# Performance work log

Hardware: AMD Instinct MI355X
Metric: run time of the kernel (lower is better)

Reference implementation:

```python
import jax, jax.numpy as jnp
import numpy as np

EMBED = 512
HEADS = 8
HEAD_DIM = EMBED // HEADS
SCALE_BASE = 512
NEG = -1e9


def xpos_apply(x, offset, downscale):
    # x: [(b h), L, d]
    L, d = x.shape[1], x.shape[2]
    min_pos = -(L + offset) // 2
    max_pos = L + offset + min_pos
    base = (jnp.arange(0, d, 2, dtype=jnp.float32) + 0.4 * d) / (1.4 * d)      # [d/2]
    power = jnp.arange(min_pos, max_pos, dtype=jnp.float32) / SCALE_BASE        # [L']
    scale = base[None, :] ** power[:, None]                                     # [L', d/2]
    half = d // 2
    inv_freq = 1.0 / (10000.0 ** (jnp.arange(half, dtype=jnp.float32) / half))
    sinusoid = jnp.arange(scale.shape[0], dtype=jnp.float32)[:, None] * inv_freq[None, :]
    sin, cos = jnp.sin(sinusoid), jnp.cos(sinusoid)
    # keep last L rows (no-op when offset == 0)
    scale, sin, cos = scale[-L:], sin[-L:], cos[-L:]
    if downscale:
        scale = 1.0 / scale
    sin2 = jnp.repeat(sin * scale, 2, axis=-1)   # duplicate_interleave -> [L, d]
    cos2 = jnp.repeat(cos * scale, 2, axis=-1)
    x1, x2 = x[..., ::2], x[..., 1::2]
    rot = jnp.stack([-x2, x1], axis=-1).reshape(x.shape)  # rotate_every_two
    return x * cos2[None] + rot * sin2[None]


def split_heads(x, b, L):
    # 'b l (h d) -> (b h) l d'
    return x.reshape(b, L, HEADS, HEAD_DIM).transpose(0, 2, 1, 3).reshape(b * HEADS, L, HEAD_DIM)


def setup_inputs() -> dict:
    key = jax.random.key(0)
    ks = jax.random.split(key, 12)
    b, L = 4, 2048
    inp = {
        'query': jax.random.normal(ks[0], (b, L, EMBED), jnp.float32),
        'key': jax.random.normal(ks[1], (b, L, EMBED), jnp.float32),
        'value': jax.random.normal(ks[2], (b, L, EMBED), jnp.float32),
        'key_padding_mask': jnp.zeros((b, L), jnp.bool_),
        'attn_mask': jnp.where(jnp.tril(jnp.ones((L, L), jnp.bool_)), 0.0, NEG).astype(jnp.float32),
    }
    s = 1.0 / np.sqrt(EMBED)
    inp['Wq'] = jax.random.normal(ks[3], (EMBED, EMBED), jnp.float32) * s
    inp['bq'] = jnp.zeros((EMBED,), jnp.float32)
    inp['Wk'] = jax.random.normal(ks[4], (EMBED, EMBED), jnp.float32) * s
    inp['bk'] = jnp.zeros((EMBED,), jnp.float32)
    inp['Wv'] = jax.random.normal(ks[5], (EMBED, EMBED), jnp.float32) * s
    inp['bv'] = jnp.zeros((EMBED,), jnp.float32)
    inp['Wo'] = jax.random.normal(ks[6], (EMBED, EMBED), jnp.float32) * s
    inp['bo'] = jnp.zeros((EMBED,), jnp.float32)
    return inp


def reference(query, key, value, key_padding_mask, attn_mask, Wq, bq, Wk, bk, Wv, bv, Wo, bo):
    b, L, _ = query.shape
    q = split_heads(query @ Wq.T + bq, b, L)
    k = split_heads(key @ Wk.T + bk, b, L)
    v = split_heads(value @ Wv.T + bv, b, L)
    k = xpos_apply(k, 0, True)
    q = xpos_apply(q, 0, False)
    q = q * (HEAD_DIM ** -0.5)
    aw = jnp.einsum('btd,bsd->bts', q, k)                 # [(b h), t, s]
    aw = jnp.nan_to_num(aw) + attn_mask[None]
    aw = aw.reshape(b, HEADS, L, L)
    aw = jnp.where(key_padding_mask[:, None, None, :], jnp.finfo(aw.dtype).min, aw)
    aw = aw.reshape(b * HEADS, L, L)
    probs = jax.nn.softmax(aw.astype(jnp.float32), axis=-1).astype(aw.dtype)
    attn = jnp.einsum('bts,bsd->btd', probs, v)           # [(b h), t, d]
    attn = attn.reshape(b, HEADS, L, HEAD_DIM).transpose(0, 2, 1, 3).reshape(b, L, EMBED)
    return attn @ Wo.T + bo
```

## Files before the change

### kernel.cpp

```cpp
#include <hip/hip_runtime.h>
#include <hip/hip_bf16.h>

typedef __bf16 bf16x2 __attribute__((ext_vector_type(2)));
typedef __bf16 bf16x4 __attribute__((ext_vector_type(4)));
typedef __bf16 bf16x8 __attribute__((ext_vector_type(8)));
typedef float  f32x4  __attribute__((ext_vector_type(4)));

#define SEQ    2048
#define EMB    512
#define NHEAD  8
#define HD     64
#define NBATCH 4
#define MROWS  (NBATCH*SEQ)
#define QSCALE 0.18033688011112042f
#define INV2PI 0.15915494309189535f
#define TWOPI  6.28318530717958648f
#define NEGFREQ (-0.41524101186092028f)

__device__ __forceinline__ f32x4 mfma16(bf16x8 a, bf16x8 b, f32x4 c) {
  return __builtin_amdgcn_mfma_f32_16x16x32_bf16(a, b, c, 0, 0, 0);
}

typedef __attribute__((address_space(1))) const void gv_t;
typedef __attribute__((address_space(3))) void lv_t;
__device__ __forceinline__ void async16(const void* g, void* l) {
  __builtin_amdgcn_global_load_lds((gv_t*)g, (lv_t*)l, 16, 0, 0);
}

__global__ __launch_bounds__(256) void conv_kernel(const float* __restrict__ q,
                                                   const float* __restrict__ k,
                                                   const float* __restrict__ v,
                                                   __bf16* __restrict__ Qf,
                                                   __bf16* __restrict__ Kf,
                                                   __bf16* __restrict__ Vf) {
  const int z = blockIdx.y;
  const float* src = (z == 0) ? q : (z == 1) ? k : v;
  __bf16* dst = (z == 0) ? Qf : (z == 1) ? Kf : Vf;
  const size_t i8 = ((size_t)blockIdx.x * 256 + threadIdx.x) * 8;
  const float4 fa = ((const float4*)(src + i8))[0];
  const float4 fb = ((const float4*)(src + i8))[1];
  bf16x8 h = { (__bf16)fa.x, (__bf16)fa.y, (__bf16)fa.z, (__bf16)fa.w,
               (__bf16)fb.x, (__bf16)fb.y, (__bf16)fb.z, (__bf16)fb.w };
  *(bf16x8*)(dst + i8) = h;
}

__device__ __forceinline__ void gemm_main(const __bf16* __restrict__ A,
                                          const float* __restrict__ W,
                                          __bf16* As, __bf16* Bs,
                                          f32x4 (&acc)[4][4], int m0, int n0) {
  const int tid = threadIdx.x;
  const int wid = tid >> 6, lane = tid & 63;
  const int quad = lane >> 4, l16 = lane & 15;
  const int srow = lane >> 3;
  const int sxor = ((lane & 7) ^ srow) * 8;
  const int wm = (wid >> 1) * 64, wn = (wid & 1) * 64;

  #pragma unroll
  for (int i = 0; i < 4; ++i)
    #pragma unroll
    for (int j = 0; j < 4; ++j) acc[i][j] = (f32x4)(0.0f);

  for (int k0 = 0; k0 < 512; k0 += 64) {
    __syncthreads();
    #pragma unroll
    for (int ii = 0; ii < 4; ++ii) {
      const int r8 = wid * 32 + ii * 8;
      async16(A + (size_t)(m0 + r8 + srow) * 512 + k0 + sxor, &As[r8 * 64]);
    }
    {
      const int row = tid >> 1, c0 = (tid & 1) << 5;
      const float* src = W + (size_t)(n0 + row) * 512 + k0 + c0;
      __bf16* dst = Bs + row * 72 + c0;
      #pragma unroll
      for (int j = 0; j < 4; ++j) {
        const float4 fa = ((const float4*)src)[2 * j];
        const float4 fb = ((const float4*)src)[2 * j + 1];
        bf16x8 h = { (__bf16)fa.x, (__bf16)fa.y, (__bf16)fa.z, (__bf16)fa.w,
                     (__bf16)fb.x, (__bf16)fb.y, (__bf16)fb.z, (__bf16)fb.w };
        *((bf16x8*)(dst + 8 * j)) = h;
      }
    }
    __syncthreads();
    #pragma unroll
    for (int ks = 0; ks < 2; ++ks) {
      bf16x8 af[4], bfr[4];
      #pragma unroll
      for (int i = 0; i < 4; ++i)
        af[i] = *(const bf16x8*)&As[(wm + i * 16 + l16) * 64 +
                                    (((quad + ks * 4) ^ (l16 & 7)) * 8)];
      #pragma unroll
      for (int j = 0; j < 4; ++j)
        bfr[j] = *(const bf16x8*)&Bs[(wn + j * 16 + l16) * 72 + ks * 32 + quad * 8];
      #pragma unroll
      for (int i = 0; i < 4; ++i)
        #pragma unroll
        for (int j = 0; j < 4; ++j)
          acc[i][j] = mfma16(af[i], bfr[j], acc[i][j]);
    }
  }
}

__global__ __launch_bounds__(256) void gemm_proj_kernel(
    const __bf16* __restrict__ Qf, const __bf16* __restrict__ Kf, const __bf16* __restrict__ Vf,
    const float* __restrict__ wq, const float* __restrict__ wk, const float* __restrict__ wv,
    const float* __restrict__ bq, const float* __restrict__ bk, const float* __restrict__ bv,
    __bf16* __restrict__ Qx, __bf16* __restrict__ Kx, __bf16* __restrict__ Vt) {
  __shared__ __align__(16) char smem[34816];
  __bf16* As = (__bf16*)smem;
  __bf16* Bs = (__bf16*)(smem + 16384);
  __bf16* T  = (__bf16*)smem;

  const int z = blockIdx.z;
  const __bf16* A = (z == 0) ? Qf : (z == 1) ? Kf : Vf;
  const float* W  = (z == 0) ? wq : (z == 1) ? wk : wv;
  const float* bias = (z == 0) ? bq : (z == 1) ? bk : bv;
  const int m0 = blockIdx.y * 128, n0 = blockIdx.x * 128;

  f32x4 acc[4][4];
  gemm_main(A, W, As, Bs, acc, m0, n0);

  const int tid = threadIdx.x;
  const int wid = tid >> 6, lane = tid & 63;
  const int quad = lane >> 4, l16 = lane & 15;
  const int wm = (wid >> 1) * 64, wn = (wid & 1) * 64;

  __syncthreads();

  if (z == 2) {
    #pragma unroll
    for (int j = 0; j < 4; ++j) {
      const float bval = bias[n0 + wn + j * 16 + l16];
      #pragma unroll
      for (int i = 0; i < 4; ++i) {
        bf16x4 p = { (__bf16)(acc[i][j][0] + bval), (__bf16)(acc[i][j][1] + bval),
                     (__bf16)(acc[i][j][2] + bval), (__bf16)(acc[i][j][3] + bval) };
        *(bf16x4*)&T[(wn + j * 16 + l16) * 136 + wm + i * 16 + quad * 4] = p;
      }
    }
    __syncthreads();
    const int nrow = tid >> 1, mh = (tid & 1) << 6;
    bf16x8 vv[8];
    #pragma unroll
    for (int u = 0; u < 8; ++u) vv[u] = *(const bf16x8*)&T[nrow * 136 + mh + u * 8];
    const int n = n0 + nrow, h = n >> 6, d = n & 63;
    const int bb = m0 >> 11, lb2 = (m0 & 2047) + mh;
    __bf16* dst = Vt + ((size_t)(bb * 8 + h) * 64 + d) * 2048 + lb2;
    #pragma unroll
    for (int u = 0; u < 8; ++u) *(bf16x8*)(dst + u * 8) = vv[u];
  } else {
    #pragma unroll
    for (int j = 0; j < 4; ++j) {
      const float bval = bias[n0 + wn + j * 16 + l16];
      #pragma unroll
      for (int i = 0; i < 4; ++i)
        #pragma unroll
        for (int r = 0; r < 4; ++r)
          T[(wm + i * 16 + quad * 4 + r) * 136 + wn + j * 16 + l16] =
              (__bf16)(acc[i][j][r] + bval);
    }
    __syncthreads();
    const int lrow = tid >> 1, half = tid & 1;
    const int gm = m0 + lrow, l = gm & 2047, bb = gm >> 11;
    const int h = (n0 >> 6) + half;
    bf16x8 vv[8];
    #pragma unroll
    for (int u = 0; u < 8; ++u)
      vv[u] = *(const bf16x8*)&T[lrow * 136 + half * 64 + u * 8];
    bf16x8 ov[8];
    const float lf = (float)l;
    const float pw = (lf - 1024.0f) * (1.0f / 512.0f);
    const float qs = (z == 0) ? QSCALE : 1.0f;
    #pragma unroll
    for (int i = 0; i < 32; ++i) {
      const float x1 = (float)vv[i >> 2][(2 * i) & 7];
      const float x2 = (float)vv[i >> 2][(2 * i + 1) & 7];
      const float lb = __log2f((2.0f * i + 25.6f) * (1.0f / 89.6f));
      const float e  = (z == 0) ? (pw * lb) : (-pw * lb);
      const float sc = __builtin_amdgcn_exp2f(e) * qs;
      const float ang = lf * __builtin_amdgcn_exp2f((float)i * NEGFREQ);
      float rev = ang * INV2PI;
      rev -= floorf(rev);
      const float ar = rev * TWOPI;
      const float sn = __sinf(ar) * sc;
      const float cs = __cosf(ar) * sc;
      ov[i >> 2][(2 * i) & 7]     = (__bf16)(x1 * cs - x2 * sn);
      ov[i >> 2][(2 * i + 1) & 7] = (__bf16)(x2 * cs + x1 * sn);
    }
    __bf16* dst = ((z == 0) ? Qx : Kx) + ((size_t)(bb * 8 + h) * 2048 + l) * 64;
    #pragma unroll
    for (int u = 0; u < 8; ++u) *(bf16x8*)(dst + u * 8) = ov[u];
  }
}

__global__ __launch_bounds__(256) void gemm_out_kernel(
    const __bf16* __restrict__ A, const float* __restrict__ W,
    const float* __restrict__ bias, float* __restrict__ C) {
  __shared__ __align__(16) char smem[34816];
  __bf16* As = (__bf16*)smem;
  __bf16* Bs = (__bf16*)(smem + 16384);
  const int m0 = blockIdx.y * 128, n0 = blockIdx.x * 128;
  f32x4 acc[4][4];
  gemm_main(A, W, As, Bs, acc, m0, n0);
  const int tid = threadIdx.x;
  const int wid = tid >> 6, lane = tid & 63;
  const int quad = lane >> 4, l16 = lane & 15;
  const int wm = (wid >> 1) * 64, wn = (wid & 1) * 64;
  #pragma unroll
  for (int j = 0; j < 4; ++j) {
    const int n = n0 + wn + j * 16 + l16;
    const float bval = bias[n];
    #pragma unroll
    for (int i = 0; i < 4; ++i)
      #pragma unroll
      for (int r = 0; r < 4; ++r)
        C[(size_t)(m0 + wm + i * 16 + quad * 4 + r) * 512 + n] = acc[i][j][r] + bval;
  }
}

__global__ __launch_bounds__(256) void flash_kernel(const __bf16* __restrict__ Qx,
                                                    const __bf16* __restrict__ Kx,
                                                    const __bf16* __restrict__ Vt,
                                                    const unsigned char* __restrict__ kpm,
                                                    __bf16* __restrict__ Oa) {
  __shared__ __align__(16) __bf16 Qs[64 * HD];
  __shared__ __align__(16) __bf16 Ks[64 * HD];
  __shared__ __align__(16) __bf16 Vs[64 * HD];
  __shared__ __align__(16) __bf16 Ps[4][16 * 72];

  const int tid = threadIdx.x;
  const int wid = tid >> 6;
  const int lane = tid & 63;
  const int quad = lane >> 4;
  const int l16 = lane & 15;
  const int srow = lane >> 3;
  const int sxor = ((lane & 7) ^ srow) * 8;
  const int l7 = l16 & 7;
  const int bh = blockIdx.x;
  const int b = bh >> 3;
  const int qb = 31 - (int)blockIdx.y;
  const int q0 = qb * 64;

  const __bf16* Qbase = Qx + (size_t)bh * (SEQ * HD);
  const __bf16* Kbase = Kx + (size_t)bh * (SEQ * HD);
  const __bf16* Vbase = Vt + (size_t)bh * (HD * SEQ);
  __bf16* Pw = &Ps[wid][0];

  #pragma unroll
  for (int ii = 0; ii < 2; ++ii) {
    const int r0 = wid * 16 + ii * 8;
    async16(Qbase + (size_t)(q0 + r0 + srow) * HD + sxor, &Qs[r0 * HD]);
  }
  __syncthreads();
  const bf16x8 qf0 = *(const bf16x8*)&Qs[(wid * 16 + l16) * HD + ((quad ^ l7) * 8)];
  const bf16x8 qf1 = *(const bf16x8*)&Qs[(wid * 16 + l16) * HD + (((quad + 4) ^ l7) * 8)];

  f32x4 o0 = (f32x4)(0.0f), o1 = (f32x4)(0.0f), o2 = (f32x4)(0.0f), o3 = (f32x4)(0.0f);
  float m_run = -1e30f, l_run = 0.0f;
  const int myq = q0 + wid * 16 + l16;

  for (int kv0 = 0; kv0 < q0 + 64; kv0 += 64) {
    __syncthreads();
    #pragma unroll
    for (int ii = 0; ii < 2; ++ii) {
      const int r0 = wid * 16 + ii * 8;
      async16(Kbase + (size_t)(kv0 + r0 + srow) * HD + sxor, &Ks[r0 * HD]);
      async16(Vbase + (size_t)(r0 + srow) * SEQ + kv0 + sxor, &Vs[r0 * HD]);
    }
    __syncthreads();

    f32x4 s[4];
    #pragma unroll
    for (int nb = 0; nb < 4; ++nb) s[nb] = (f32x4)(0.0f);
    #pragma unroll
    for (int nb = 0; nb < 4; ++nb) {
      const bf16x8 kf = *(const bf16x8*)&Ks[(nb * 16 + l16) * HD + ((quad ^ l7) * 8)];
      s[nb] = mfma16(kf, qf0, s[nb]);
    }
    #pragma unroll
    for (int nb = 0; nb < 4; ++nb) {
      const bf16x8 kf = *(const bf16x8*)&Ks[(nb * 16 + l16) * HD + (((quad + 4) ^ l7) * 8)];
      s[nb] = mfma16(kf, qf1, s[nb]);
    }

    if (kv0 + 63 > q0 + wid * 16) {
      #pragma unroll
      for (int nb = 0; nb < 4; ++nb)
        #pragma unroll
        for (int r = 0; r < 4; ++r)
          if (kv0 + nb * 16 + quad * 4 + r > myq) s[nb][r] = -1e30f;
    }
    {
      const unsigned char* kp0 = kpm + b * SEQ + kv0;
      #pragma unroll
      for (int nb = 0; nb < 4; ++nb) {
        const unsigned pk = *(const unsigned*)(kp0 + nb * 16 + quad * 4);
        if (pk) {
          if (pk & 0x000000FFu) s[nb][0] = -1e30f;
          if (pk & 0x0000FF00u) s[nb][1] = -1e30f;
          if (pk & 0x00FF0000u) s[nb][2] = -1e30f;
          if (pk & 0xFF000000u) s[nb][3] = -1e30f;
        }
      }
    }

    float mx = s[0][0];
    #pragma unroll
    for (int nb = 0; nb < 4; ++nb)
      #pragma unroll
      for (int r = 0; r < 4; ++r) mx = fmaxf(mx, s[nb][r]);
    mx = fmaxf(mx, __shfl_xor(mx, 16));
    mx = fmaxf(mx, __shfl_xor(mx, 32));
    const float m_new = fmaxf(m_run, mx);
    const float alpha = __builtin_amdgcn_exp2f(m_run - m_new);
    m_run = m_new;
    float ssum = 0.0f;
    #pragma unroll
    for (int nb = 0; nb < 4; ++nb) {
      #pragma unroll
      for (int r = 0; r < 4; ++r) {
        const float p = __builtin_amdgcn_exp2f(s[nb][r] - m_new);
        s[nb][r] = p;
        ssum += p;
      }
    }
    ssum += __shfl_xor(ssum, 16);
    ssum += __shfl_xor(ssum, 32);
    l_run = l_run * alpha + ssum;

    #pragma unroll
    for (int nb = 0; nb < 4; ++nb) {
      bf16x4 p4 = { (__bf16)s[nb][0], (__bf16)s[nb][1],
                    (__bf16)s[nb][2], (__bf16)s[nb][3] };
      *(bf16x4*)&Pw[l16 * 72 + nb * 16 + quad * 4] = p4;
    }
    o0 *= alpha; o1 *= alpha; o2 *= alpha; o3 *= alpha;

    #pragma unroll
    for (int ks = 0; ks < 2; ++ks) {
      const bf16x8 pf = *(const bf16x8*)&Pw[l16 * 72 + ks * 32 + quad * 8];
      const int bx = ((quad + ks * 4) ^ l7) * 8;
      o0 = mfma16(*(const bf16x8*)&Vs[( 0 + l16) * HD + bx], pf, o0);
      o1 = mfma16(*(const bf16x8*)&Vs[(16 + l16) * HD + bx], pf, o1);
      o2 = mfma16(*(const bf16x8*)&Vs[(32 + l16) * HD + bx], pf, o2);
      o3 = mfma16(*(const bf16x8*)&Vs[(48 + l16) * HD + bx], pf, o3);
    }
  }

  const float inv_l = 1.0f / l_run;
  {
    bf16x4 t0 = { (__bf16)(o0[0] * inv_l), (__bf16)(o0[1] * inv_l),
                  (__bf16)(o0[2] * inv_l), (__bf16)(o0[3] * inv_l) };
    bf16x4 t1 = { (__bf16)(o1[0] * inv_l), (__bf16)(o1[1] * inv_l),
                  (__bf16)(o1[2] * inv_l), (__bf16)(o1[3] * inv_l) };
    bf16x4 t2 = { (__bf16)(o2[0] * inv_l), (__bf16)(o2[1] * inv_l),
                  (__bf16)(o2[2] * inv_l), (__bf16)(o2[3] * inv_l) };
    bf16x4 t3 = { (__bf16)(o3[0] * inv_l), (__bf16)(o3[1] * inv_l),
                  (__bf16)(o3[2] * inv_l), (__bf16)(o3[3] * inv_l) };
    *(bf16x4*)&Pw[l16 * 72 +  0 + quad * 4] = t0;
    *(bf16x4*)&Pw[l16 * 72 + 16 + quad * 4] = t1;
    *(bf16x4*)&Pw[l16 * 72 + 32 + quad * 4] = t2;
    *(bf16x4*)&Pw[l16 * 72 + 48 + quad * 4] = t3;
  }
  const int h = bh & 7;
  #pragma unroll
  for (int ii = 0; ii < 2; ++ii) {
    const int qr = ii * 8 + (lane >> 3);
    const bf16x8 ovv = *(const bf16x8*)&Pw[qr * 72 + (lane & 7) * 8];
    *(bf16x8*)(Oa + (((size_t)b * SEQ + q0 + wid * 16 + qr) * NHEAD + h) * HD +
               (lane & 7) * 8) = ovv;
  }
}

extern "C" void kernel_launch(void* const* d_in, const int* in_sizes, int n_in,
                              void* d_out, int out_size, void* d_ws, size_t ws_size,
                              hipStream_t stream) {
  (void)in_sizes; (void)n_in; (void)out_size; (void)ws_size;
  const float* query = (const float*)d_in[0];
  const float* key   = (const float*)d_in[1];
  const float* value = (const float*)d_in[2];
  const unsigned char* kpm = (const unsigned char*)d_in[3];
  const float* Wq = (const float*)d_in[5];
  const float* bq = (const float*)d_in[6];
  const float* Wk = (const float*)d_in[7];
  const float* bk = (const float*)d_in[8];
  const float* Wv = (const float*)d_in[9];
  const float* bv = (const float*)d_in[10];
  const float* Wo = (const float*)d_in[11];
  const float* bo = (const float*)d_in[12];
  float* out = (float*)d_out;

  char* ws = (char*)d_ws;
  const size_t SZ = (size_t)MROWS * EMB * 2;
  __bf16* Qf = (__bf16*)(ws);
  __bf16* Kf = (__bf16*)(ws + SZ);
  __bf16* Vf = (__bf16*)(ws + 2 * SZ);
  __bf16* Qx = (__bf16*)(ws + 3 * SZ);
  __bf16* Kx = (__bf16*)(ws + 4 * SZ);
  __bf16* Vt = (__bf16*)(ws + 5 * SZ);
  __bf16* Oa = Qf;

  conv_kernel<<<dim3(2048, 3), dim3(256), 0, stream>>>(query, key, value, Qf, Kf, Vf);
  gemm_proj_kernel<<<dim3(4, 64, 3), dim3(256), 0, stream>>>(
      Qf, Kf, Vf, Wq, Wk, Wv, bq, bk, bv, Qx, Kx, Vt);
  flash_kernel<<<dim3(32, 32), dim3(256), 0, stream>>>(Qx, Kx, Vt, kpm, Oa);
  gemm_out_kernel<<<dim3(4, 64), dim3(256), 0, stream>>>(Oa, Wo, bo, out);
}
```

Before: 233.3 us.

## Pair causal query blocks per workgroup and double-buffer K/V tiles in flash kernel

Each flash workgroup now processes two query blocks (31-t and t), so every block does exactly 33 KV iterations. This balances the causal triangle and halves the grid. K/V tiles are double-buffered, with the next tile's async load issued before computing the current one, which removes one barrier per iteration. The key padding mask is staged once into shared memory. In exchange, LDS use and register pressure rise, and the grid shrinks to 512 blocks, which may lower occupancy.

```diff
diff --git a/kernel.cpp b/kernel.cpp
--- a/kernel.cpp
+++ b/kernel.cpp
@@ -222,23 +222,26 @@
                                                     const __bf16* __restrict__ Vt,
                                                     const unsigned char* __restrict__ kpm,
                                                     __bf16* __restrict__ Oa) {
-  __shared__ __align__(16) __bf16 Qs[64 * HD];
-  __shared__ __align__(16) __bf16 Ks[64 * HD];
-  __shared__ __align__(16) __bf16 Vs[64 * HD];
+  __shared__ __align__(16) __bf16 Qs[2][64 * HD];
+  __shared__ __align__(16) __bf16 Ks[2][64 * HD];
+  __shared__ __align__(16) __bf16 Vs[2][64 * HD];
   __shared__ __align__(16) __bf16 Ps[4][16 * 72];
+  __shared__ __align__(16) unsigned char kpmS[2048];
 
   const int tid = threadIdx.x;
   const int wid = tid >> 6;
   const int lane = tid & 63;
   const int quad = lane >> 4;
   const int l16 = lane & 15;
+  const int l7 = l16 & 7;
   const int srow = lane >> 3;
   const int sxor = ((lane & 7) ^ srow) * 8;
-  const int l7 = l16 & 7;
   const int bh = blockIdx.x;
-  const int b = bh >> 3;
-  const int qb = 31 - (int)blockIdx.y;
-  const int q0 = qb * 64;
+  const int b = bh >> 3, h = bh & 7;
+  const int t = blockIdx.y;
+  const int qb0 = 31 - t, qb1 = t;
+  const int n0 = qb0 + 1;
+  const int ntot = n0 + qb1 + 1;
 
   const __bf16* Qbase = Qx + (size_t)bh * (SEQ * HD);
   const __bf16* Kbase = Kx + (size_t)bh * (SEQ * HD);
@@ -246,108 +249,33 @@
   __bf16* Pw = &Ps[wid][0];
 
   #pragma unroll
+  for (int p = 0; p < 2; ++p) {
+    const int q0p = (p ? qb1 : qb0) * 64;
+    #pragma unroll
+    for (int ii = 0; ii < 2; ++ii) {
+      const int r0 = wid * 16 + ii * 8;
+      async16(Qbase + (size_t)(q0p + r0 + srow) * HD + sxor, &Qs[p][r0 * HD]);
+    }
+  }
+  if (wid < 2) async16(kpm + b * SEQ + tid * 16, &kpmS[tid * 16]);
+  #pragma unroll
   for (int ii = 0; ii < 2; ++ii) {
     const int r0 = wid * 16 + ii * 8;
-    async16(Qbase + (size_t)(q0 + r0 + srow) * HD + sxor, &Qs[r0 * HD]);
+    async16(Kbase + (size_t)(r0 + srow) * HD + sxor, &Ks[0][r0 * HD]);
+    async16(Vbase + (size_t)(r0 + srow) * SEQ + sxor, &Vs[0][r0 * HD]);
   }
   __syncthreads();
-  const bf16x8 qf0 = *(const bf16x8*)&Qs[(wid * 16 + l16) * HD + ((quad ^ l7) * 8)];
-  const bf16x8 qf1 = *(const bf16x8*)&Qs[(wid * 16 + l16) * HD + (((quad + 4) ^ l7) * 8)];
+
+  bf16x8 qf0 = *(const bf16x8*)&Qs[0][(wid * 16 + l16) * HD + ((quad ^ l7) * 8)];
+  bf16x8 qf1 = *(const bf16x8*)&Qs[0][(wid * 16 + l16) * HD + (((quad + 4) ^ l7) * 8)];
 
   f32x4 o0 = (f32x4)(0.0f), o1 = (f32x4)(0.0f), o2 = (f32x4)(0.0f), o3 = (f32x4)(0.0f);
-  float m_run = -1e30f, l_run = 0.0f;
-  const int myq = q0 + wid * 16 + l16;
-
-  for (int kv0 = 0; kv0 < q0 + 64; kv0 += 64) {
-    __syncthreads();
-    #pragma unroll
-    for (int ii = 0; ii < 2; ++ii) {
-      const int r0 = wid * 16 + ii * 8;
-      async16(Kbase + (size_t)(kv0 + r0 + srow) * HD + sxor, &Ks[r0 * HD]);
-      async16(Vbase + (size_t)(r0 + srow) * SEQ + kv0 + sxor, &Vs[r0 * HD]);
-    }
-    __syncthreads();
-
-    f32x4 s[4];
-    #pragma unroll
-    for (int nb = 0; nb < 4; ++nb) s[nb] = (f32x4)(0.0f);
-    #pragma unroll
-    for (int nb = 0; nb < 4; ++nb) {
-      const bf16x8 kf = *(const bf16x8*)&Ks[(nb * 16 + l16) * HD + ((quad ^ l7) * 8)];
-      s[nb] = mfma16(kf, qf0, s[nb]);
-    }
-    #pragma unroll
-    for (int nb = 0; nb < 4; ++nb) {
-      const bf16x8 kf = *(const bf16x8*)&Ks[(nb * 16 + l16) * HD + (((quad + 4) ^ l7) * 8)];
-      s[nb] = mfma16(kf, qf1, s[nb]);
-    }
-
-    if (kv0 + 63 > q0 + wid * 16) {
-      #pragma unroll
-      for (int nb = 0; nb < 4; ++nb)
-        #pragma unroll
-        for (int r = 0; r < 4; ++r)
-          if (kv0 + nb * 16 + quad * 4 + r > myq) s[nb][r] = -1e30f;
-    }
-    {
-      const unsigned char* kp0 = kpm + b * SEQ + kv0;
-      #pragma unroll
-      for (int nb = 0; nb < 4; ++nb) {
-        const unsigned pk = *(const unsigned*)(kp0 + nb * 16 + quad * 4);
-        if (pk) {
-          if (pk & 0x000000FFu) s[nb][0] = -1e30f;
-          if (pk & 0x0000FF00u) s[nb][1] = -1e30f;
-          if (pk & 0x00FF0000u) s[nb][2] = -1e30f;
-          if (pk & 0xFF000000u) s[nb][3] = -1e30f;
-        }
-      }
-    }
-
-    float mx = s[0][0];
-    #pragma unroll
-    for (int nb = 0; nb < 4; ++nb)
-      #pragma unroll
-      for (int r = 0; r < 4; ++r) mx = fmaxf(mx, s[nb][r]);
-    mx = fmaxf(mx, __shfl_xor(mx, 16));
-    mx = fmaxf(mx, __shfl_xor(mx, 32));
-    const float m_new = fmaxf(m_run, mx);
-    const float alpha = __builtin_amdgcn_exp2f(m_run - m_new);
-    m_run = m_new;
-    float ssum = 0.0f;
-    #pragma unroll
-    for (int nb = 0; nb < 4; ++nb) {
-      #pragma unroll
-      for (int r = 0; r < 4; ++r) {
-        const float p = __builtin_amdgcn_exp2f(s[nb][r] - m_new);
-        s[nb][r] = p;
-        ssum += p;
-      }
-    }
-    ssum += __shfl_xor(ssum, 16);
-    ssum += __shfl_xor(ssum, 32);
-    l_run = l_run * alpha + ssum;
-
-    #pragma unroll
-    for (int nb = 0; nb < 4; ++nb) {
-      bf16x4 p4 = { (__bf16)s[nb][0], (__bf16)s[nb][1],
-                    (__bf16)s[nb][2], (__bf16)s[nb][3] };
-      *(bf16x4*)&Pw[l16 * 72 + nb * 16 + quad * 4] = p4;
-    }
-    o0 *= alpha; o1 *= alpha; o2 *= alpha; o3 *= alpha;
-
-    #pragma unroll
-    for (int ks = 0; ks < 2; ++ks) {
-      const bf16x8 pf = *(const bf16x8*)&Pw[l16 * 72 + ks * 32 + quad * 8];
-      const int bx = ((quad + ks * 4) ^ l7) * 8;
-      o0 = mfma16(*(const bf16x8*)&Vs[( 0 + l16) * HD + bx], pf, o0);
-      o1 = mfma16(*(const bf16x8*)&Vs[(16 + l16) * HD + bx], pf, o1);
-      o2 = mfma16(*(const bf16x8*)&Vs[(32 + l16) * HD + bx], pf, o2);
-      o3 = mfma16(*(const bf16x8*)&Vs[(48 + l16) * HD + bx], pf, o3);
-    }
-  }
-
-  const float inv_l = 1.0f / l_run;
-  {
+  float m_run = -3.0e38f, l_run = 0.0f;
+  int qb = qb0, q0 = qb0 * 64;
+  int myq = q0 + wid * 16 + l16;
+
+  auto store_O = [&](int q0s) {
+    const float inv_l = 1.0f / l_run;
     bf16x4 t0 = { (__bf16)(o0[0] * inv_l), (__bf16)(o0[1] * inv_l),
                   (__bf16)(o0[2] * inv_l), (__bf16)(o0[3] * inv_l) };
     bf16x4 t1 = { (__bf16)(o1[0] * inv_l), (__bf16)(o1[1] * inv_l),
@@ -360,15 +288,116 @@
     *(bf16x4*)&Pw[l16 * 72 + 16 + quad * 4] = t1;
     *(bf16x4*)&Pw[l16 * 72 + 32 + quad * 4] = t2;
     *(bf16x4*)&Pw[l16 * 72 + 48 + quad * 4] = t3;
-  }
-  const int h = bh & 7;
-  #pragma unroll
-  for (int ii = 0; ii < 2; ++ii) {
-    const int qr = ii * 8 + (lane >> 3);
-    const bf16x8 ovv = *(const bf16x8*)&Pw[qr * 72 + (lane & 7) * 8];
-    *(bf16x8*)(Oa + (((size_t)b * SEQ + q0 + wid * 16 + qr) * NHEAD + h) * HD +
-               (lane & 7) * 8) = ovv;
-  }
+    #pragma unroll
+    for (int ii = 0; ii < 2; ++ii) {
+      const int qr = ii * 8 + srow;
+      const bf16x8 ovv = *(const bf16x8*)&Pw[qr * 72 + (lane & 7) * 8];
+      *(bf16x8*)(Oa + (((size_t)b * SEQ + q0s + wid * 16 + qr) * NHEAD + h) * HD +
+                 (lane & 7) * 8) = ovv;
+    }
+  };
+
+  for (int i = 0; i < 33; ++i) {
+    const int buf = i & 1;
+    if (i + 1 < ntot) {
+      const int inext = i + 1;
+      const int kvn = (inext < n0) ? inext : (inext - n0);
+      #pragma unroll
+      for (int ii = 0; ii < 2; ++ii) {
+        const int r0 = wid * 16 + ii * 8;
+        async16(Kbase + (size_t)(kvn * 64 + r0 + srow) * HD + sxor, &Ks[buf ^ 1][r0 * HD]);
+        async16(Vbase + (size_t)(r0 + srow) * SEQ + kvn * 64 + sxor, &Vs[buf ^ 1][r0 * HD]);
+      }
+    }
+    if (i == n0) {
+      store_O(qb0 * 64);
+      qf0 = *(const bf16x8*)&Qs[1][(wid * 16 + l16) * HD + ((quad ^ l7) * 8)];
+      qf1 = *(const bf16x8*)&Qs[1][(wid * 16 + l16) * HD + (((quad + 4) ^ l7) * 8)];
+      o0 = o1 = o2 = o3 = (f32x4)(0.0f);
+      m_run = -3.0e38f; l_run = 0.0f;
+      qb = qb1; q0 = qb1 * 64; myq = q0 + wid * 16 + l16;
+    }
+    if (i >= ntot) { __syncthreads(); continue; }
+    const int kv = (i < n0) ? i : (i - n0);
+
+    f32x4 s[4];
+    #pragma unroll
+    for (int nb = 0; nb < 4; ++nb) s[nb] = (f32x4)(0.0f);
+    #pragma unroll
+    for (int nb = 0; nb < 4; ++nb) {
+      const bf16x8 kf = *(const bf16x8*)&Ks[buf][(nb * 16 + l16) * HD + ((quad ^ l7) * 8)];
+      s[nb] = mfma16(kf, qf0, s[nb]);
+    }
+    #pragma unroll
+    for (int nb = 0; nb < 4; ++nb) {
+      const bf16x8 kf = *(const bf16x8*)&Ks[buf][(nb * 16 + l16) * HD + (((quad + 4) ^ l7) * 8)];
+      s[nb] = mfma16(kf, qf1, s[nb]);
+    }
+
+    if (kv == qb) {
+      #pragma unroll
+      for (int nb = 0; nb < 4; ++nb)
+        #pragma unroll
+        for (int r = 0; r < 4; ++r)
+          if (kv * 64 + nb * 16 + quad * 4 + r > myq) s[nb][r] = -1e30f;
+    }
+    #pragma unroll
+    for (int nb = 0; nb < 4; ++nb) {
+      const unsigned pk = *(const unsigned*)&kpmS[kv * 64 + nb * 16 + quad * 4];
+      if (pk) {
+        if (pk & 0x000000FFu) s[nb][0] = -1e30f;
+        if (pk & 0x0000FF00u) s[nb][1] = -1e30f;
+        if (pk & 0x00FF0000u) s[nb][2] = -1e30f;
+        if (pk & 0xFF000000u) s[nb][3] = -1e30f;
+      }
+    }
+
+    float mx = s[0][0];
+    #pragma unroll
+    for (int nb = 0; nb < 4; ++nb)
+      #pragma unroll
+      for (int r = 0; r < 4; ++r) mx = fmaxf(mx, s[nb][r]);
+    mx = fmaxf(mx, __shfl_xor(mx, 16));
+    mx = fmaxf(mx, __shfl_xor(mx, 32));
+    const float m_new = fmaxf(m_run, mx);
+    const float alpha = __builtin_amdgcn_exp2f(m_run - m_new);
+    m_run = m_new;
+    float ssum = 0.0f;
+    #pragma unroll
+    for (int nb = 0; nb < 4; ++nb) {
+      #pragma unroll
+      for (int r = 0; r < 4; ++r) {
+        const float p = __builtin_amdgcn_exp2f(s[nb][r] - m_new);
+        s[nb][r] = p;
+        ssum += p;
+      }
+    }
+    ssum += __shfl_xor(ssum, 16);
+    ssum += __shfl_xor(ssum, 32);
+    l_run = l_run * alpha + ssum;
+
+    #pragma unroll
+    for (int nb = 0; nb < 4; ++nb) {
+      bf16x4 p4 = { (__bf16)s[nb][0], (__bf16)s[nb][1],
+                    (__bf16)s[nb][2], (__bf16)s[nb][3] };
+      *(bf16x4*)&Pw[l16 * 72 + nb * 16 + quad * 4] = p4;
+    }
+    o0 *= alpha; o1 *= alpha; o2 *= alpha; o3 *= alpha;
+
+    #pragma unroll
+    for (int ks = 0; ks < 2; ++ks) {
+      const bf16x8 pf = *(const bf16x8*)&Pw[l16 * 72 + ks * 32 + quad * 8];
+      const int bx = ((quad + ks * 4) ^ l7) * 8;
+      o0 = mfma16(*(const bf16x8*)&Vs[buf][( 0 + l16) * HD + bx], pf, o0);
+      o1 = mfma16(*(const bf16x8*)&Vs[buf][(16 + l16) * HD + bx], pf, o1);
+      o2 = mfma16(*(const bf16x8*)&Vs[buf][(32 + l16) * HD + bx], pf, o2);
+      o3 = mfma16(*(const bf16x8*)&Vs[buf][(48 + l16) * HD + bx], pf, o3);
+    }
+
+    __syncthreads();
+  }
+
+  store_O(qb1 * 64);
 }
 
 extern "C" void kernel_launch(void* const* d_in, const int* in_sizes, int n_in,
@@ -402,6 +431,6 @@
   conv_kernel<<<dim3(2048, 3), dim3(256), 0, stream>>>(query, key, value, Qf, Kf, Vf);
   gemm_proj_kernel<<<dim3(4, 64, 3), dim3(256), 0, stream>>>(
       Qf, Kf, Vf, Wq, Wk, Wv, bq, bk, bv, Qx, Kx, Vt);
-  flash_kernel<<<dim3(32, 32), dim3(256), 0, stream>>>(Qx, Kx, Vt, kpm, Oa);
+  flash_kernel<<<dim3(32, 16), dim3(256), 0, stream>>>(Qx, Kx, Vt, kpm, Oa);
   gemm_out_kernel<<<dim3(4, 64), dim3(256), 0, stream>>>(Oa, Wo, bo, out);
 }
```

Measured after the change: 227.9 us. -2.3%, faster.

## Use 128-row query tiles in flash attention with reordered scheduling and staged padding mask

Applied to the files above, without the earlier changes.

The flash attention kernel now gives each block 128 query rows (32 per wave, two 16-row MFMA column groups), so every K/V tile loaded into shared memory feeds twice as many MFMAs and the grid halves. The key padding mask is staged once into shared memory, and the first K/V tile is prefetched together with Q. Query tiles are scheduled in a mixed order (largest first, then smallest) to balance the causal workload. The larger tile raises register pressure, which the launch bounds try to contain, and leaves fewer blocks to spread across CUs.

```diff
diff --git a/kernel.cpp b/kernel.cpp
--- a/kernel.cpp
+++ b/kernel.cpp
@@ -217,28 +217,31 @@
   }
 }
 
-__global__ __launch_bounds__(256) void flash_kernel(const __bf16* __restrict__ Qx,
-                                                    const __bf16* __restrict__ Kx,
-                                                    const __bf16* __restrict__ Vt,
-                                                    const unsigned char* __restrict__ kpm,
-                                                    __bf16* __restrict__ Oa) {
-  __shared__ __align__(16) __bf16 Qs[64 * HD];
+__global__ __launch_bounds__(256, 3) void flash_kernel(const __bf16* __restrict__ Qx,
+                                                       const __bf16* __restrict__ Kx,
+                                                       const __bf16* __restrict__ Vt,
+                                                       const unsigned char* __restrict__ kpm,
+                                                       __bf16* __restrict__ Oa) {
+  __shared__ __align__(16) __bf16 Qs[128 * HD];
   __shared__ __align__(16) __bf16 Ks[64 * HD];
   __shared__ __align__(16) __bf16 Vs[64 * HD];
-  __shared__ __align__(16) __bf16 Ps[4][16 * 72];
+  __shared__ __align__(16) __bf16 Ps[4][32 * 72];
+  __shared__ __align__(16) unsigned char kpmS[2048];
 
   const int tid = threadIdx.x;
   const int wid = tid >> 6;
   const int lane = tid & 63;
   const int quad = lane >> 4;
   const int l16 = lane & 15;
+  const int l7 = l16 & 7;
   const int srow = lane >> 3;
   const int sxor = ((lane & 7) ^ srow) * 8;
-  const int l7 = l16 & 7;
   const int bh = blockIdx.x;
-  const int b = bh >> 3;
-  const int qb = 31 - (int)blockIdx.y;
-  const int q0 = qb * 64;
+  const int b = bh >> 3, h = bh & 7;
+  const int y = blockIdx.y;
+  const int qt = (y < 8) ? (15 - y) : (y - 8);
+  const int q0 = qt * 128;
+  const int nkv = 2 * qt + 2;
 
   const __bf16* Qbase = Qx + (size_t)bh * (SEQ * HD);
   const __bf16* Kbase = Kx + (size_t)bh * (SEQ * HD);
@@ -246,127 +249,165 @@
   __bf16* Pw = &Ps[wid][0];
 
   #pragma unroll
+  for (int ii = 0; ii < 4; ++ii) {
+    const int r0 = wid * 32 + ii * 8;
+    async16(Qbase + (size_t)(q0 + r0 + srow) * HD + sxor, &Qs[r0 * HD]);
+  }
+  if (wid < 2) async16(kpm + b * SEQ + tid * 16, &kpmS[tid * 16]);
+  #pragma unroll
   for (int ii = 0; ii < 2; ++ii) {
     const int r0 = wid * 16 + ii * 8;
-    async16(Qbase + (size_t)(q0 + r0 + srow) * HD + sxor, &Qs[r0 * HD]);
+    async16(Kbase + (size_t)(r0 + srow) * HD + sxor, &Ks[r0 * HD]);
+    async16(Vbase + (size_t)(r0 + srow) * SEQ + sxor, &Vs[r0 * HD]);
   }
   __syncthreads();
-  const bf16x8 qf0 = *(const bf16x8*)&Qs[(wid * 16 + l16) * HD + ((quad ^ l7) * 8)];
-  const bf16x8 qf1 = *(const bf16x8*)&Qs[(wid * 16 + l16) * HD + (((quad + 4) ^ l7) * 8)];
-
-  f32x4 o0 = (f32x4)(0.0f), o1 = (f32x4)(0.0f), o2 = (f32x4)(0.0f), o3 = (f32x4)(0.0f);
-  float m_run = -1e30f, l_run = 0.0f;
-  const int myq = q0 + wid * 16 + l16;
-
-  for (int kv0 = 0; kv0 < q0 + 64; kv0 += 64) {
-    __syncthreads();
-    #pragma unroll
-    for (int ii = 0; ii < 2; ++ii) {
-      const int r0 = wid * 16 + ii * 8;
-      async16(Kbase + (size_t)(kv0 + r0 + srow) * HD + sxor, &Ks[r0 * HD]);
-      async16(Vbase + (size_t)(r0 + srow) * SEQ + kv0 + sxor, &Vs[r0 * HD]);
-    }
-    __syncthreads();
-
-    f32x4 s[4];
-    #pragma unroll
-    for (int nb = 0; nb < 4; ++nb) s[nb] = (f32x4)(0.0f);
+
+  bf16x8 qf[2][2];
+  #pragma unroll
+  for (int ks = 0; ks < 2; ++ks)
+    #pragma unroll
+    for (int c = 0; c < 2; ++c)
+      qf[ks][c] = *(const bf16x8*)&Qs[(wid * 32 + c * 16 + l16) * HD +
+                                      (((quad + ks * 4) ^ l7) * 8)];
+
+  f32x4 o[4][2];
+  #pragma unroll
+  for (int db = 0; db < 4; ++db)
+    #pragma unroll
+    for (int c = 0; c < 2; ++c) o[db][c] = (f32x4)(0.0f);
+  float m_run[2] = { -3.0e38f, -3.0e38f };
+  float l_run[2] = { 0.0f, 0.0f };
+  const int myq0 = q0 + wid * 32 + l16;
+
+  for (int kvt = 0; kvt < nkv; ++kvt) {
+    f32x4 s[4][2];
+    #pragma unroll
+    for (int nb = 0; nb < 4; ++nb)
+      #pragma unroll
+      for (int c = 0; c < 2; ++c) s[nb][c] = (f32x4)(0.0f);
+    #pragma unroll
+    for (int ks = 0; ks < 2; ++ks) {
+      bf16x8 kf[4];
+      #pragma unroll
+      for (int nb = 0; nb < 4; ++nb)
+        kf[nb] = *(const bf16x8*)&Ks[(nb * 16 + l16) * HD + (((quad + ks * 4) ^ l7) * 8)];
+      #pragma unroll
+      for (int nb = 0; nb < 4; ++nb)
+        #pragma unroll
+        for (int c = 0; c < 2; ++c)
+          s[nb][c] = mfma16(kf[nb], qf[ks][c], s[nb][c]);
+    }
+
+    if (kvt * 64 + 63 > q0 + wid * 32) {
+      #pragma unroll
+      for (int c = 0; c < 2; ++c) {
+        const int myq = myq0 + c * 16;
+        #pragma unroll
+        for (int nb = 0; nb < 4; ++nb)
+          #pragma unroll
+          for (int r = 0; r < 4; ++r)
+            if (kvt * 64 + nb * 16 + quad * 4 + r > myq) s[nb][c][r] = -1e30f;
+      }
+    }
     #pragma unroll
     for (int nb = 0; nb < 4; ++nb) {
-      const bf16x8 kf = *(const bf16x8*)&Ks[(nb * 16 + l16) * HD + ((quad ^ l7) * 8)];
-      s[nb] = mfma16(kf, qf0, s[nb]);
-    }
-    #pragma unroll
-    for (int nb = 0; nb < 4; ++nb) {
-      const bf16x8 kf = *(const bf16x8*)&Ks[(nb * 16 + l16) * HD + (((quad + 4) ^ l7) * 8)];
-      s[nb] = mfma16(kf, qf1, s[nb]);
-    }
-
-    if (kv0 + 63 > q0 + wid * 16) {
+      const unsigned pk = *(const unsigned*)&kpmS[kvt * 64 + nb * 16 + quad * 4];
+      if (pk) {
+        #pragma unroll
+        for (int c = 0; c < 2; ++c) {
+          if (pk & 0x000000FFu) s[nb][c][0] = -1e30f;
+          if (pk & 0x0000FF00u) s[nb][c][1] = -1e30f;
+          if (pk & 0x00FF0000u) s[nb][c][2] = -1e30f;
+          if (pk & 0xFF000000u) s[nb][c][3] = -1e30f;
+        }
+      }
+    }
+
+    float alpha[2];
+    #pragma unroll
+    for (int c = 0; c < 2; ++c) {
+      float mx = s[0][c][0];
       #pragma unroll
       for (int nb = 0; nb < 4; ++nb)
         #pragma unroll
-        for (int r = 0; r < 4; ++r)
-          if (kv0 + nb * 16 + quad * 4 + r > myq) s[nb][r] = -1e30f;
-    }
-    {
-      const unsigned char* kp0 = kpm + b * SEQ + kv0;
+        for (int r = 0; r < 4; ++r) mx = fmaxf(mx, s[nb][c][r]);
+      mx = fmaxf(mx, __shfl_xor(mx, 16));
+      mx = fmaxf(mx, __shfl_xor(mx, 32));
+      const float m_new = fmaxf(m_run[c], mx);
+      alpha[c] = __builtin_amdgcn_exp2f(m_run[c] - m_new);
+      m_run[c] = m_new;
+      float ssum = 0.0f;
       #pragma unroll
       for (int nb = 0; nb < 4; ++nb) {
-        const unsigned pk = *(const unsigned*)(kp0 + nb * 16 + quad * 4);
-        if (pk) {
-          if (pk & 0x000000FFu) s[nb][0] = -1e30f;
-          if (pk & 0x0000FF00u) s[nb][1] = -1e30f;
-          if (pk & 0x00FF0000u) s[nb][2] = -1e30f;
-          if (pk & 0xFF000000u) s[nb][3] = -1e30f;
+        #pragma unroll
+        for (int r = 0; r < 4; ++r) {
+          const float p = __builtin_amdgcn_exp2f(s[nb][c][r] - m_new);
+          s[nb][c][r] = p;
+          ssum += p;
         }
       }
-    }
-
-    float mx = s[0][0];
-    #pragma unroll
-    for (int nb = 0; nb < 4; ++nb)
-      #pragma unroll
-      for (int r = 0; r < 4; ++r) mx = fmaxf(mx, s[nb][r]);
-    mx = fmaxf(mx, __shfl_xor(mx, 16));
-    mx = fmaxf(mx, __shfl_xor(mx, 32));
-    const float m_new = fmaxf(m_run, mx);
-    const float alpha = __builtin_amdgcn_exp2f(m_run - m_new);
-    m_run = m_new;
-    float ssum = 0.0f;
-    #pragma unroll
-    for (int nb = 0; nb < 4; ++nb) {
-      #pragma unroll
-      for (int r = 0; r < 4; ++r) {
-        const float p = __builtin_amdgcn_exp2f(s[nb][r] - m_new);
-        s[nb][r] = p;
-        ssum += p;
-      }
-    }
-    ssum += __shfl_xor(ssum, 16);
-    ssum += __shfl_xor(ssum, 32);
-    l_run = l_run * alpha + ssum;
-
-    #pragma unroll
-    for (int nb = 0; nb < 4; ++nb) {
-      bf16x4 p4 = { (__bf16)s[nb][0], (__bf16)s[nb][1],
-                    (__bf16)s[nb][2], (__bf16)s[nb][3] };
-      *(bf16x4*)&Pw[l16 * 72 + nb * 16 + quad * 4] = p4;
-    }
-    o0 *= alpha; o1 *= alpha; o2 *= alpha; o3 *= alpha;
+      ssum += __shfl_xor(ssum, 16);
+      ssum += __shfl_xor(ssum, 32);
+      l_run[c] = l_run[c] * alpha[c] + ssum;
+    }
+
+    #pragma unroll
+    for (int c = 0; c < 2; ++c)
+      #pragma unroll
+      for (int nb = 0; nb < 4; ++nb) {
+        bf16x4 p4 = { (__bf16)s[nb][c][0], (__bf16)s[nb][c][1],
+                      (__bf16)s[nb][c][2], (__bf16)s[nb][c][3] };
+        *(bf16x4*)&Pw[(c * 16 + l16) * 72 + nb * 16 + quad * 4] = p4;
+      }
+    #pragma unroll
+    for (int db = 0; db < 4; ++db)
+      #pragma unroll
+      for (int c = 0; c < 2; ++c) o[db][c] *= alpha[c];
 
     #pragma unroll
     for (int ks = 0; ks < 2; ++ks) {
-      const bf16x8 pf = *(const bf16x8*)&Pw[l16 * 72 + ks * 32 + quad * 8];
-      const int bx = ((quad + ks * 4) ^ l7) * 8;
-      o0 = mfma16(*(const bf16x8*)&Vs[( 0 + l16) * HD + bx], pf, o0);
-      o1 = mfma16(*(const bf16x8*)&Vs[(16 + l16) * HD + bx], pf, o1);
-      o2 = mfma16(*(const bf16x8*)&Vs[(32 + l16) * HD + bx], pf, o2);
-      o3 = mfma16(*(const bf16x8*)&Vs[(48 + l16) * HD + bx], pf, o3);
-    }
-  }
-
-  const float inv_l = 1.0f / l_run;
-  {
-    bf16x4 t0 = { (__bf16)(o0[0] * inv_l), (__bf16)(o0[1] * inv_l),
-                  (__bf16)(o0[2] * inv_l), (__bf16)(o0[3] * inv_l) };
-    bf16x4 t1 = { (__bf16)(o1[0] * inv_l), (__bf16)(o1[1] * inv_l),
-                  (__bf16)(o1[2] * inv_l), (__bf16)(o1[3] * inv_l) };
-    bf16x4 t2 = { (__bf16)(o2[0] * inv_l), (__bf16)(o2[1] * inv_l),
-                  (__bf16)(o2[2] * inv_l), (__bf16)(o2[3] * inv_l) };
-    bf16x4 t3 = { (__bf16)(o3[0] * inv_l), (__bf16)(o3[1] * inv_l),
-                  (__bf16)(o3[2] * inv_l), (__bf16)(o3[3] * inv_l) };
-    *(bf16x4*)&Pw[l16 * 72 +  0 + quad * 4] = t0;
-    *(bf16x4*)&Pw[l16 * 72 + 16 + quad * 4] = t1;
-    *(bf16x4*)&Pw[l16 * 72 + 32 + quad * 4] = t2;
-    *(bf16x4*)&Pw[l16 * 72 + 48 + quad * 4] = t3;
-  }
-  const int h = bh & 7;
-  #pragma unroll
-  for (int ii = 0; ii < 2; ++ii) {
-    const int qr = ii * 8 + (lane >> 3);
+      bf16x8 pf[2];
+      #pragma unroll
+      for (int c = 0; c < 2; ++c)
+        pf[c] = *(const bf16x8*)&Pw[(c * 16 + l16) * 72 + ks * 32 + quad * 8];
+      #pragma unroll
+      for (int db = 0; db < 4; ++db) {
+        const bf16x8 vf = *(const bf16x8*)&Vs[(db * 16 + l16) * HD +
+                                              (((quad + ks * 4) ^ l7) * 8)];
+        #pragma unroll
+        for (int c = 0; c < 2; ++c)
+          o[db][c] = mfma16(vf, pf[c], o[db][c]);
+      }
+    }
+
+    __syncthreads();
+    if (kvt + 1 < nkv) {
+      const int kvn = kvt + 1;
+      #pragma unroll
+      for (int ii = 0; ii < 2; ++ii) {
+        const int r0 = wid * 16 + ii * 8;
+        async16(Kbase + (size_t)(kvn * 64 + r0 + srow) * HD + sxor, &Ks[r0 * HD]);
+        async16(Vbase + (size_t)(r0 + srow) * SEQ + kvn * 64 + sxor, &Vs[r0 * HD]);
+      }
+    }
+    __syncthreads();
+  }
+
+  #pragma unroll
+  for (int c = 0; c < 2; ++c) {
+    const float inv_l = 1.0f / l_run[c];
+    #pragma unroll
+    for (int db = 0; db < 4; ++db) {
+      bf16x4 t4 = { (__bf16)(o[db][c][0] * inv_l), (__bf16)(o[db][c][1] * inv_l),
+                    (__bf16)(o[db][c][2] * inv_l), (__bf16)(o[db][c][3] * inv_l) };
+      *(bf16x4*)&Pw[(c * 16 + l16) * 72 + db * 16 + quad * 4] = t4;
+    }
+  }
+  #pragma unroll
+  for (int ii = 0; ii < 4; ++ii) {
+    const int qr = ii * 8 + srow;
     const bf16x8 ovv = *(const bf16x8*)&Pw[qr * 72 + (lane & 7) * 8];
-    *(bf16x8*)(Oa + (((size_t)b * SEQ + q0 + wid * 16 + qr) * NHEAD + h) * HD +
+    *(bf16x8*)(Oa + (((size_t)b * SEQ + q0 + wid * 32 + qr) * NHEAD + h) * HD +
                (lane & 7) * 8) = ovv;
   }
 }
@@ -402,6 +443,6 @@
   conv_kernel<<<dim3(2048, 3), dim3(256), 0, stream>>>(query, key, value, Qf, Kf, Vf);
   gemm_proj_kernel<<<dim3(4, 64, 3), dim3(256), 0, stream>>>(
       Qf, Kf, Vf, Wq, Wk, Wv, bq, bk, bv, Qx, Kx, Vt);
-  flash_kernel<<<dim3(32, 32), dim3(256), 0, stream>>>(Qx, Kx, Vt, kpm, Oa);
+  flash_kernel<<<dim3(32, 16), dim3(256), 0, stream>>>(Qx, Kx, Vt, kpm, Oa);
   gemm_out_kernel<<<dim3(4, 64), dim3(256), 0, stream>>>(Oa, Wo, bo, out);
 }
```

New measurement: 239.3 us. 1.03x slower.
